# Optimization experiments

Measured on AMD Instinct MI355X. Metric: run time of the kernel, lower is better.

## Reference

```python
import jax, jax.numpy as jnp
import numpy as np

N, E, G = 100000, 1600000, 128
IN_DIM, H, C = 329, 4, 64
NEG_SLOPE = 0.2


def setup_inputs() -> dict:
    key = jax.random.key(0)
    ks = jax.random.split(key, 12)
    x = jax.random.normal(ks[0], (N, IN_DIM), dtype=jnp.float32)
    edge_index = jax.random.randint(ks[1], (2, E), 0, N, dtype=jnp.int64)
    batch = jnp.sort(jax.random.randint(ks[2], (N,), 0, G, dtype=jnp.int64))
    s = 1.0 / np.sqrt(IN_DIM)
    W = jax.random.uniform(ks[3], (IN_DIM, H * C), jnp.float32, -s, s)
    att_src = jax.random.normal(ks[4], (H, C), dtype=jnp.float32) * 0.1
    att_dst = jax.random.normal(ks[5], (H, C), dtype=jnp.float32) * 0.1
    bias = jnp.zeros((C,), jnp.float32)
    s1 = 1.0 / np.sqrt(C)
    w1 = jax.random.uniform(ks[6], (C, 64), jnp.float32, -s1, s1)
    b1 = jnp.zeros((64,), jnp.float32)
    s2 = 1.0 / np.sqrt(64)
    w2 = jax.random.uniform(ks[7], (64, 1), jnp.float32, -s2, s2)
    b2 = jnp.zeros((1,), jnp.float32)
    return {"x": x, "W": W, "att_src": att_src, "att_dst": att_dst,
            "bias": bias, "w1": w1, "b1": b1, "w2": w2, "b2": b2,
            "edge_index": edge_index, "batch": batch}


def reference(x, W, att_src, att_dst, bias, w1, b1, w2, b2, edge_index, batch):
    # --- GATConv (heads=4, concat=False, add_self_loops=True) ---
    xp = (x @ W).reshape(N, H, C)                       # [N,H,C]
    a_src = jnp.einsum('nhc,hc->nh', xp, att_src)       # [N,H]
    a_dst = jnp.einsum('nhc,hc->nh', xp, att_dst)       # [N,H]
    loops = jnp.arange(N, dtype=edge_index.dtype)
    src = jnp.concatenate([edge_index[0], loops])       # [E+N]
    dst = jnp.concatenate([edge_index[1], loops])
    logits = jax.nn.leaky_relu(a_src[src] + a_dst[dst], NEG_SLOPE)  # [E+N,H]
    # segment softmax over edges sharing a destination
    mx = jax.ops.segment_max(logits, dst, num_segments=N)
    ex = jnp.exp(logits - mx[dst])
    denom = jax.ops.segment_sum(ex, dst, num_segments=N)
    alpha = ex / denom[dst]                             # [E+N,H]
    msg = xp[src] * alpha[:, :, None]                   # [E+N,H,C]
    agg = jax.ops.segment_sum(msg, dst, num_segments=N) # [N,H,C]
    h = jax.nn.relu(agg.mean(axis=1) + bias)            # [N,C]
    # --- global mean pool over graphs ---
    counts = jax.ops.segment_sum(jnp.ones((N,), h.dtype), batch, num_segments=G)
    g = jax.ops.segment_sum(h, batch, num_segments=G) / jnp.maximum(counts, 1.0)[:, None]
    # --- head MLP ---
    y = jax.nn.sigmoid(jax.nn.relu(g @ w1 + b1) @ w2 + b2)  # [G,1]
    return y
```

## Files before the change

### kernel.cpp

```cpp
#include <hip/hip_runtime.h>
#include <math.h>

#define N_NODES 100000
#define N_EDGES 1600000
#define N_GRAPHS 128
#define IN_DIM 329
#define NH 4
#define CC 64
#define HC 256
#define NEG_SLOPE 0.2f
#define LOG2E 1.44269504f

#define K_PAD 384
#define M_PAD 100096
#define XBYTES (N_NODES * IN_DIM * 4)
#define NBUCK 196
#define BCAP 10240
#define EPB 8192

typedef unsigned short u16;
typedef unsigned char u8;
typedef unsigned int u32;
typedef __attribute__((ext_vector_type(8))) short short8;
typedef __attribute__((ext_vector_type(4))) float floatx4;
typedef __attribute__((ext_vector_type(2))) float floatx2;

__device__ __forceinline__ u16 f2bf(float f) {
    u32 u = __float_as_uint(f);
    u32 r = (u + 0x7FFFu + ((u >> 16) & 1u)) >> 16;
    return (u16)r;
}

__device__ __forceinline__ u32 pkbf(float a, float b) {
    return __builtin_amdgcn_perm(__float_as_uint(b), __float_as_uint(a), 0x07060302u);
}

__device__ __forceinline__ u8 f2fp8(float f) {
#if __has_builtin(__builtin_amdgcn_cvt_pk_fp8_f32)
    int pk = __builtin_amdgcn_cvt_pk_fp8_f32(f, f, 0, false);
    return (u8)(pk & 0xFF);
#else
    u32 u = __float_as_uint(f);
    u32 sgn = (u >> 24) & 0x80;
    float af = fabsf(f);
    if (af >= 448.f) return (u8)(sgn | 0x7E);
    if (af < 0.015625f) {
        int m = (int)rintf(af * 512.f);
        if (m >= 8) return (u8)(sgn | 0x08);
        return (u8)(sgn | (u32)m);
    }
    u32 au = u & 0x7FFFFFFF;
    u32 r = au + 0x0007FFFFu + ((au >> 20) & 1u);
    u32 e = r >> 23;
    u32 m3 = (r >> 20) & 7;
    int fe = (int)e - 127 + 7;
    if (fe >= 16) return (u8)(sgn | 0x7E);
    return (u8)(sgn | ((u32)fe << 3) | m3);
#endif
}

__device__ __forceinline__ float fp82f_sw(u32 b) {
    u32 s = (b & 0x80u) << 24;
    u32 e = (b >> 3) & 0xF;
    u32 m = b & 7;
    if (e == 0) {
        float v = (float)m * 0.001953125f;
        return (b & 0x80) ? -v : v;
    }
    return __uint_as_float(s | ((e + 120) << 23) | (m << 20));
}

__device__ __forceinline__ floatx4 dec4(int p) {
#if __has_builtin(__builtin_amdgcn_cvt_pk_f32_fp8)
    floatx2 lo = __builtin_amdgcn_cvt_pk_f32_fp8(p, false);
    floatx2 hi = __builtin_amdgcn_cvt_pk_f32_fp8(p, true);
    floatx4 r; r.x = lo.x; r.y = lo.y; r.z = hi.x; r.w = hi.y;
    return r;
#else
    floatx4 r;
    r.x = fp82f_sw(p & 0xFF);  r.y = fp82f_sw((p >> 8) & 0xFF);
    r.z = fp82f_sw((p >> 16) & 0xFF); r.w = fp82f_sw((p >> 24) & 0xFF);
    return r;
#endif
}

__device__ __forceinline__ void async_copy16(const void* g, void* l) {
    __builtin_amdgcn_global_load_lds((const __attribute__((address_space(1))) void*)g,
                                     (__attribute__((address_space(3))) void*)l, 16, 0, 0);
}

__global__ __launch_bounds__(256) void convw_kernel(const float* __restrict__ W, u16* __restrict__ WbT)
{
    int i = blockIdx.x * 256 + threadIdx.x;
    if (i >= HC * 96) return;
    int c = i / 96;
    int k0 = (i - c * 96) * 4;
    ushort4 o = {0, 0, 0, 0};
    const float* wp = W + c;
    if (k0 < IN_DIM)     o.x = f2bf(wp[(size_t)k0 * HC]);
    if (k0 + 1 < IN_DIM) o.y = f2bf(wp[(size_t)(k0 + 1) * HC]);
    if (k0 + 2 < IN_DIM) o.z = f2bf(wp[(size_t)(k0 + 2) * HC]);
    if (k0 + 3 < IN_DIM) o.w = f2bf(wp[(size_t)(k0 + 3) * HC]);
    *(ushort4*)(WbT + (size_t)c * K_PAD + k0) = o;
}

__global__ __launch_bounds__(512, 6) void gemm_mfma_kernel(
    const float* __restrict__ x, const u16* __restrict__ WbT, u8* __restrict__ xp8)
{
    __shared__ __align__(16) float Asf[64 * 64];
    __shared__ __align__(16) u16   Bs[256 * 64];

    const int tid = threadIdx.x;
    const int lane = tid & 63;
    const int wave = tid >> 6;
    const int lr = lane & 15;
    const int q = lane >> 4;
    const int row0 = blockIdx.x * 64;
    const int rm0 = (wave & 1) * 32;
    const int cn0 = (wave >> 1) * 64;

    floatx4 acc[2][4];
#pragma unroll
    for (int i = 0; i < 2; i++)
#pragma unroll
        for (int j = 0; j < 4; j++) {
            acc[i][j].x = 0.f; acc[i][j].y = 0.f; acc[i][j].z = 0.f; acc[i][j].w = 0.f;
        }

    for (int k0 = 0; k0 < K_PAD; k0 += 64) {
#pragma unroll
        for (int t = 0; t < 2; t++) {
            int chunk = tid + t * 512;
            int row = chunk >> 4, ch = chunk & 15;
            int chl = ch ^ (row & 15);
            long gb = (long)(row0 + row) * (IN_DIM * 4) + (long)k0 * 4 + chl * 16;
            if (gb > (long)XBYTES - 16) gb = (long)XBYTES - 16;
            async_copy16((const char*)x + gb, (char*)Asf + (size_t)chunk * 16);
        }
#pragma unroll
        for (int t = 0; t < 4; t++) {
            int off = (tid + t * 512) * 16;
            int rowb = off >> 7;
            int colb = off & 127;
            int gcol = colb ^ ((rowb & 7) * 16);
            const char* gb = (const char*)WbT + (size_t)rowb * (K_PAD * 2) + k0 * 2 + gcol;
            async_copy16(gb, (char*)Bs + off);
        }
        asm volatile("s_waitcnt vmcnt(0)" ::: "memory");
        __syncthreads();

#pragma unroll
        for (int ks = 0; ks < 2; ks++) {
            short8 af[2], bf[4];
#pragma unroll
            for (int i = 0; i < 2; i++) {
                int ra = rm0 + i * 16 + lr;
                int c0 = ks * 8 + q * 2;
                int sw = ra & 15;
                const float4* base = (const float4*)(Asf + ra * 64);
                float4 lo = base[c0 ^ sw];
                float4 hi = base[(c0 ^ sw) ^ 1];
                union { short8 v; u32 w[4]; } fr;
                fr.w[0] = pkbf(lo.x, lo.y);
                fr.w[1] = pkbf(lo.z, lo.w);
                fr.w[2] = pkbf(hi.x, hi.y);
                fr.w[3] = pkbf(hi.z, hi.w);
                af[i] = fr.v;
            }
#pragma unroll
            for (int j = 0; j < 4; j++) {
                int rb = cn0 + j * 16 + lr;
                int cb = (ks * 64 + q * 16) ^ ((rb & 7) * 16);
                bf[j] = *(const short8*)((const char*)Bs + rb * 128 + cb);
            }
#pragma unroll
            for (int i = 0; i < 2; i++)
#pragma unroll
                for (int j = 0; j < 4; j++)
                    acc[i][j] = __builtin_amdgcn_mfma_f32_16x16x32_bf16(af[i], bf[j], acc[i][j], 0, 0, 0);
        }
        __syncthreads();
    }

#pragma unroll
    for (int i = 0; i < 2; i++) {
#pragma unroll
        for (int j = 0; j < 4; j++) {
            int col = cn0 + j * 16 + lr;
            float v[4] = {acc[i][j].x, acc[i][j].y, acc[i][j].z, acc[i][j].w};
#pragma unroll
            for (int r = 0; r < 4; r++) {
                int row = row0 + rm0 + i * 16 + q * 4 + r;
                if (row < N_NODES) xp8[(size_t)row * HC + col] = f2fp8(v[r]);
            }
        }
    }
}

__global__ __launch_bounds__(256) void a8_kernel(
    const u8* __restrict__ xp8, const float* __restrict__ att_src, const float* __restrict__ att_dst,
    float* __restrict__ a_src, float* __restrict__ a_dst)
{
    int n = blockIdx.x * 4 + (threadIdx.x >> 6);
    int lane = threadIdx.x & 63;
    if (n >= N_NODES) return;
    int h = lane >> 4;
    int c0 = (lane & 15) * 4;
    int p = *(const int*)(xp8 + (size_t)n * HC + h * CC + c0);
    floatx4 v = dec4(p);
    const float* as = att_src + h * CC + c0;
    const float* ad = att_dst + h * CC + c0;
    float ps = v.x * as[0] + v.y * as[1] + v.z * as[2] + v.w * as[3];
    float pd = v.x * ad[0] + v.y * ad[1] + v.z * ad[2] + v.w * ad[3];
#pragma unroll
    for (int m = 1; m < 16; m <<= 1) {
        ps += __shfl_xor(ps, m, 64);
        pd += __shfl_xor(pd, m, 64);
    }
    if ((lane & 15) == 0) {
        a_src[n * 4 + h] = ps * LOG2E;
        a_dst[n * 4 + h] = pd * LOG2E;
    }
}

__global__ __launch_bounds__(256) void bin2_kernel(
    const int* __restrict__ ei, int* __restrict__ bcur, int2* __restrict__ bins)
{
    __shared__ int hist[NBUCK];
    __shared__ int gpos[NBUCK];
    __shared__ int lcur[NBUCK];
    __shared__ int sc[256];

    const int t = threadIdx.x;
    const int lo = blockIdx.x * EPB;
    const int hi = min(lo + EPB, N_EDGES + N_NODES);

    for (int b = t; b < NBUCK; b += 256) hist[b] = 0;
    __syncthreads();

    for (int i = lo + t; i < hi; i += 256) {
        int d = (i < N_EDGES) ? ei[N_EDGES + i] : (i - N_EDGES);
        atomicAdd(&hist[d >> 9], 1);
    }
    __syncthreads();

    int v = (t < NBUCK) ? hist[t] : 0;
    if (t < NBUCK) { gpos[t] = atomicAdd(&bcur[t], v); lcur[t] = 0; }
    (void)sc;
    __syncthreads();

    for (int i = lo + t; i < hi; i += 256) {
        int s, d;
        if (i < N_EDGES) { s = ei[i]; d = ei[N_EDGES + i]; }
        else             { s = i - N_EDGES; d = s; }
        int b = d >> 9;
        int pos = gpos[b] + atomicAdd(&lcur[b], 1);
        if (pos < BCAP) {
            int2 r; r.x = s; r.y = d;
            bins[(size_t)b * BCAP + pos] = r;
        }
    }
}

__global__ __launch_bounds__(512) void fill3_kernel(
    const int* __restrict__ bcur, const int2* __restrict__ bins,
    int2* __restrict__ rs_deg, int* __restrict__ csr)
{
    __shared__ int deg[512];
    __shared__ int cur[512];
    __shared__ int sc[256];
    __shared__ int order[BCAP];

    const int t = threadIdx.x;
    const int b = blockIdx.x;
    const int cnt = min(bcur[b], BCAP);
    const int2* bp = bins + (size_t)b * BCAP;
    const int gbase = b * BCAP;

    deg[t] = 0;
    __syncthreads();
    for (int i = t; i < cnt; i += 512) atomicAdd(&deg[bp[i].y & 511], 1);
    __syncthreads();

    int d0 = 0, d1 = 0;
    if (t < 256) {
        d0 = deg[2 * t]; d1 = deg[2 * t + 1];
        sc[t] = d0 + d1;
    }
    __syncthreads();
    for (int off = 1; off < 256; off <<= 1) {
        int u = (t < 256 && t >= off) ? sc[t - off] : 0;
        __syncthreads();
        if (t < 256) sc[t] += u;
        __syncthreads();
    }
    if (t < 256) {
        int excl = sc[t] - (d0 + d1);
        cur[2 * t] = excl;
        cur[2 * t + 1] = excl + d0;
        int n0 = b * 512 + 2 * t;
        if (n0 < N_NODES)     { int2 rd; rd.x = gbase + excl;      rd.y = d0; rs_deg[n0] = rd; }
        if (n0 + 1 < N_NODES) { int2 rd; rd.x = gbase + excl + d0; rd.y = d1; rs_deg[n0 + 1] = rd; }
    }
    __syncthreads();

    for (int i = t; i < cnt; i += 512) {
        int2 r = bp[i];
        int pos = atomicAdd(&cur[r.y & 511], 1);
        order[pos] = r.x;
    }
    __syncthreads();

    for (int i = t; i < cnt; i += 512) csr[gbase + i] = order[i];
}

__global__ __launch_bounds__(256) void aggregate_kernel(
    const u8* __restrict__ xp8, const float* __restrict__ a_src, const float* __restrict__ a_dst,
    const int2* __restrict__ rs_deg, const int* __restrict__ csr,
    const float* __restrict__ bias, float* __restrict__ hbuf)
{
    int n = blockIdx.x * 4 + (threadIdx.x >> 6);
    int lane = threadIdx.x & 63;
    if (n >= N_NODES) return;
    int2 rd = rs_deg[n];
    int rstart = __builtin_amdgcn_readfirstlane(rd.x);
    int deg    = __builtin_amdgcn_readfirstlane(rd.y);
    const int* ep = csr + rstart;
    int h = lane >> 4;
    int xoff = lane * 4;

    float ad = a_dst[n * 4 + h];

    const int dm1 = deg - 1;
    const int nb  = (deg + 3) >> 2;

    float acc0 = 0.f, acc1 = 0.f, acc2 = 0.f, acc3 = 0.f, den = 0.f;

    int iA0, iA1, iA2, iA3;
    int iB0 = 0, iB1 = 0, iB2 = 0, iB3 = 0;
    float aa0, aa1, aa2, aa3;  int pa0, pa1, pa2, pa3;
    float ab0, ab1, ab2, ab3;  int pb0, pb1, pb2, pb3;

#define AGG_LDI(eb_, j0, j1, j2, j3) do { \
        j0 = ep[min((eb_), dm1)];     j1 = ep[min((eb_) + 1, dm1)]; \
        j2 = ep[min((eb_) + 2, dm1)]; j3 = ep[min((eb_) + 3, dm1)]; } while (0)

#define AGG_LDD(j0, j1, j2, j3, a0_, a1_, a2_, a3_, q0_, q1_, q2_, q3_) do { \
        a0_ = a_src[(size_t)(j0) * 4 + h];  q0_ = *(const int*)(xp8 + (size_t)(j0) * HC + xoff); \
        a1_ = a_src[(size_t)(j1) * 4 + h];  q1_ = *(const int*)(xp8 + (size_t)(j1) * HC + xoff); \
        a2_ = a_src[(size_t)(j2) * 4 + h];  q2_ = *(const int*)(xp8 + (size_t)(j2) * HC + xoff); \
        a3_ = a_src[(size_t)(j3) * 4 + h];  q3_ = *(const int*)(xp8 + (size_t)(j3) * HC + xoff); } while (0)

#define AGG_CMP(eb_, a0_, a1_, a2_, a3_, q0_, q1_, q2_, q3_) do { \
        float z0 = a0_ + ad, z1 = a1_ + ad, z2 = a2_ + ad, z3 = a3_ + ad; \
        float w0 = exp2f(fmaxf(z0, NEG_SLOPE * z0)); \
        float w1 = exp2f(fmaxf(z1, NEG_SLOPE * z1)); \
        float w2 = exp2f(fmaxf(z2, NEG_SLOPE * z2)); \
        float w3 = exp2f(fmaxf(z3, NEG_SLOPE * z3)); \
        if ((eb_) + 3 >= deg) {                \
            if ((eb_) + 1 >= deg) w1 = 0.f; \
            if ((eb_) + 2 >= deg) w2 = 0.f; \
            if ((eb_) + 3 >= deg) w3 = 0.f; \
        } \
        den += (w0 + w1) + (w2 + w3); \
        floatx4 v0 = dec4(q0_), v1 = dec4(q1_), v2 = dec4(q2_), v3 = dec4(q3_); \
        acc0 = fmaf(w0, v0.x, acc0); acc1 = fmaf(w0, v0.y, acc1); \
        acc2 = fmaf(w0, v0.z, acc2); acc3 = fmaf(w0, v0.w, acc3); \
        acc0 = fmaf(w1, v1.x, acc0); acc1 = fmaf(w1, v1.y, acc1); \
        acc2 = fmaf(w1, v1.z, acc2); acc3 = fmaf(w1, v1.w, acc3); \
        acc0 = fmaf(w2, v2.x, acc0); acc1 = fmaf(w2, v2.y, acc1); \
        acc2 = fmaf(w2, v2.z, acc2); acc3 = fmaf(w2, v2.w, acc3); \
        acc0 = fmaf(w3, v3.x, acc0); acc1 = fmaf(w3, v3.y, acc1); \
        acc2 = fmaf(w3, v3.z, acc2); acc3 = fmaf(w3, v3.w, acc3); } while (0)

    AGG_LDI(0, iA0, iA1, iA2, iA3);
    AGG_LDD(iA0, iA1, iA2, iA3, aa0, aa1, aa2, aa3, pa0, pa1, pa2, pa3);
    if (nb > 1) AGG_LDI(4, iB0, iB1, iB2, iB3);

    for (int b = 0; b < nb; b += 2) {
        int eb = b * 4;
        if (b + 1 < nb) AGG_LDD(iB0, iB1, iB2, iB3, ab0, ab1, ab2, ab3, pb0, pb1, pb2, pb3);
        if (b + 2 < nb) AGG_LDI(eb + 8, iA0, iA1, iA2, iA3);
        AGG_CMP(eb, aa0, aa1, aa2, aa3, pa0, pa1, pa2, pa3);
        if (b + 1 < nb) {
            if (b + 2 < nb) AGG_LDD(iA0, iA1, iA2, iA3, aa0, aa1, aa2, aa3, pa0, pa1, pa2, pa3);
            if (b + 3 < nb) AGG_LDI(eb + 12, iB0, iB1, iB2, iB3);
            AGG_CMP(eb + 4, ab0, ab1, ab2, ab3, pb0, pb1, pb2, pb3);
        }
    }

#undef AGG_LDI
#undef AGG_LDD
#undef AGG_CMP

    float r = 1.f / den;
    acc0 *= r; acc1 *= r; acc2 *= r; acc3 *= r;
#pragma unroll
    for (int m = 16; m <= 32; m <<= 1) {
        acc0 += __shfl_xor(acc0, m, 64);
        acc1 += __shfl_xor(acc1, m, 64);
        acc2 += __shfl_xor(acc2, m, 64);
        acc3 += __shfl_xor(acc3, m, 64);
    }
    if (lane < 16) {
        const float* bp = bias + lane * 4;
        float4 o;
        o.x = fmaxf(0.25f * acc0 + bp[0], 0.f);
        o.y = fmaxf(0.25f * acc1 + bp[1], 0.f);
        o.z = fmaxf(0.25f * acc2 + bp[2], 0.f);
        o.w = fmaxf(0.25f * acc3 + bp[3], 0.f);
        *(float4*)&hbuf[(size_t)n * CC + lane * 4] = o;
    }
}

__global__ __launch_bounds__(256) void pool1_kernel(
    const float* __restrict__ hbuf, const int* __restrict__ batch,
    float* __restrict__ gsum, int* __restrict__ gcnt)
{
    int w = threadIdx.x >> 6, lane = threadIdx.x & 63;
    int r0 = blockIdx.x * 128 + w * 32;
    if (r0 >= N_NODES) return;
    int r1 = min(r0 + 32, N_NODES);
    int cur = batch[r0];
    float s = 0.f;
    int c = 0;
    for (int r = r0; r < r1; r++) {
        int bb = batch[r];
        if (bb != cur) {
            atomicAdd(&gsum[cur * 64 + lane], s);
            if (lane == 0) atomicAdd(&gcnt[cur], c);
            s = 0.f; c = 0; cur = bb;
        }
        s += hbuf[(size_t)r * CC + lane];
        c++;
    }
    atomicAdd(&gsum[cur * 64 + lane], s);
    if (lane == 0) atomicAdd(&gcnt[cur], c);
}

__global__ __launch_bounds__(64) void pool2_kernel(
    const float* __restrict__ gsum, const int* __restrict__ gcnt,
    const float* __restrict__ w1, const float* __restrict__ b1,
    const float* __restrict__ w2, const float* __restrict__ b2,
    float* __restrict__ out)
{
    int g = blockIdx.x;
    int lane = threadIdx.x;
    __shared__ float gv[64];
    gv[lane] = gsum[g * 64 + lane] / (float)max(gcnt[g], 1);
    __syncthreads();
    float hid = b1[lane];
    for (int c = 0; c < 64; c++) hid = fmaf(gv[c], w1[c * 64 + lane], hid);
    hid = fmaxf(hid, 0.f);
    float part = hid * w2[lane];
#pragma unroll
    for (int off = 32; off > 0; off >>= 1) part += __shfl_xor(part, off, 64);
    if (lane == 0) out[g] = 1.f / (1.f + __expf(-(part + b2[0])));
}

extern "C" void kernel_launch(void* const* d_in, const int* in_sizes, int n_in,
                              void* d_out, int out_size, void* d_ws, size_t ws_size,
                              hipStream_t stream)
{
    const float* x       = (const float*)d_in[0];
    const float* W       = (const float*)d_in[1];
    const float* att_src = (const float*)d_in[2];
    const float* att_dst = (const float*)d_in[3];
    const float* bias    = (const float*)d_in[4];
    const float* w1      = (const float*)d_in[5];
    const float* b1      = (const float*)d_in[6];
    const float* w2      = (const float*)d_in[7];
    const float* b2      = (const float*)d_in[8];
    const int*   ei      = (const int*)d_in[9];
    const int*   batch   = (const int*)d_in[10];
    float* out = (float*)d_out;

    char* ws = (char*)d_ws;
    size_t off = 0;
    auto alloc = [&](size_t bytes) -> void* {
        void* p = ws + off;
        off += (bytes + 255) & ~(size_t)255;
        return p;
    };
    u16*   WbT       = (u16*)alloc((size_t)HC * K_PAD * 2);
    u8*    xp8       = (u8*)alloc((size_t)N_NODES * HC);
    float* a_src_b   = (float*)alloc((size_t)N_NODES * NH * 4);
    float* a_dst_b   = (float*)alloc((size_t)N_NODES * NH * 4);
    size_t zoff0 = off;
    int*   bcur      = (int*)alloc((size_t)NBUCK * 4);
    float* gsum      = (float*)alloc((size_t)N_GRAPHS * 64 * 4);
    int*   gcnt      = (int*)alloc((size_t)N_GRAPHS * 4);
    size_t zbytes = off - zoff0;
    int2*  bins      = (int2*)alloc((size_t)NBUCK * BCAP * 8);
    int2*  rs_deg    = (int2*)alloc((size_t)N_NODES * 8);
    int*   csr       = (int*)alloc((size_t)NBUCK * BCAP * 4);
    float* hbuf      = (float*)alloc((size_t)N_NODES * CC * 4);

    hipMemsetAsync(bcur, 0, zbytes, stream);

    convw_kernel<<<(HC * 96 + 255) / 256, 256, 0, stream>>>(W, WbT);

    gemm_mfma_kernel<<<M_PAD / 64, 512, 0, stream>>>(x, WbT, xp8);

    a8_kernel<<<(N_NODES + 3) / 4, 256, 0, stream>>>(xp8, att_src, att_dst, a_src_b, a_dst_b);

    int tot = N_EDGES + N_NODES;
    bin2_kernel<<<(tot + EPB - 1) / EPB, 256, 0, stream>>>(ei, bcur, bins);
    fill3_kernel<<<NBUCK, 512, 0, stream>>>(bcur, bins, rs_deg, csr);

    aggregate_kernel<<<(N_NODES + 3) / 4, 256, 0, stream>>>(xp8, a_src_b, a_dst_b,
                                                            rs_deg, csr, bias, hbuf);

    pool1_kernel<<<(N_NODES + 127) / 128, 256, 0, stream>>>(hbuf, batch, gsum, gcnt);
    pool2_kernel<<<N_GRAPHS, 64, 0, stream>>>(gsum, gcnt, w1, b1, w2, b2, out);
}
```

Baseline: 403.0 us.

## Fuse attention-score dots into GEMM epilogue and pooling into aggregation

The attention dot products are now computed from the fp32 MFMA accumulators in the GEMM epilogue, which removes the separate a8 kernel and its re-read of xp8. The aggregate kernel also does the global mean-pool sum directly: it accumulates into shared memory when all four nodes in a block share a graph, and otherwise uses global atomics. This drops the hbuf write/read and the pool1 kernel. The cost is extra shuffles and registers in the GEMM, and a block-wide sync in the aggregate kernel. The attention scores are now taken from unquantized values rather than fp8, so they shift slightly.

```diff
diff --git a/kernel.cpp b/kernel.cpp
--- a/kernel.cpp
+++ b/kernel.cpp
@@ -105,7 +105,9 @@
 }
 
 __global__ __launch_bounds__(512, 6) void gemm_mfma_kernel(
-    const float* __restrict__ x, const u16* __restrict__ WbT, u8* __restrict__ xp8)
+    const float* __restrict__ x, const u16* __restrict__ WbT, u8* __restrict__ xp8,
+    const float* __restrict__ att_src, const float* __restrict__ att_dst,
+    float* __restrict__ a_src, float* __restrict__ a_dst)
 {
     __shared__ __align__(16) float Asf[64 * 64];
     __shared__ __align__(16) u16   Bs[256 * 64];
@@ -195,31 +197,48 @@
             }
         }
     }
-}
-
-__global__ __launch_bounds__(256) void a8_kernel(
-    const u8* __restrict__ xp8, const float* __restrict__ att_src, const float* __restrict__ att_dst,
-    float* __restrict__ a_src, float* __restrict__ a_dst)
-{
-    int n = blockIdx.x * 4 + (threadIdx.x >> 6);
-    int lane = threadIdx.x & 63;
-    if (n >= N_NODES) return;
-    int h = lane >> 4;
-    int c0 = (lane & 15) * 4;
-    int p = *(const int*)(xp8 + (size_t)n * HC + h * CC + c0);
-    floatx4 v = dec4(p);
-    const float* as = att_src + h * CC + c0;
-    const float* ad = att_dst + h * CC + c0;
-    float ps = v.x * as[0] + v.y * as[1] + v.z * as[2] + v.w * as[3];
-    float pd = v.x * ad[0] + v.y * ad[1] + v.z * ad[2] + v.w * ad[3];
+
+    float as0 = att_src[cn0 + 0 * 16 + lr], ad0 = att_dst[cn0 + 0 * 16 + lr];
+    float as1 = att_src[cn0 + 1 * 16 + lr], ad1 = att_dst[cn0 + 1 * 16 + lr];
+    float as2 = att_src[cn0 + 2 * 16 + lr], ad2 = att_dst[cn0 + 2 * 16 + lr];
+    float as3 = att_src[cn0 + 3 * 16 + lr], ad3 = att_dst[cn0 + 3 * 16 + lr];
+
+    float ps[2][4], pd[2][4];
+#pragma unroll
+    for (int i = 0; i < 2; i++) {
+        ps[i][0] = acc[i][0].x * as0 + acc[i][1].x * as1 + acc[i][2].x * as2 + acc[i][3].x * as3;
+        ps[i][1] = acc[i][0].y * as0 + acc[i][1].y * as1 + acc[i][2].y * as2 + acc[i][3].y * as3;
+        ps[i][2] = acc[i][0].z * as0 + acc[i][1].z * as1 + acc[i][2].z * as2 + acc[i][3].z * as3;
+        ps[i][3] = acc[i][0].w * as0 + acc[i][1].w * as1 + acc[i][2].w * as2 + acc[i][3].w * as3;
+        pd[i][0] = acc[i][0].x * ad0 + acc[i][1].x * ad1 + acc[i][2].x * ad2 + acc[i][3].x * ad3;
+        pd[i][1] = acc[i][0].y * ad0 + acc[i][1].y * ad1 + acc[i][2].y * ad2 + acc[i][3].y * ad3;
+        pd[i][2] = acc[i][0].z * ad0 + acc[i][1].z * ad1 + acc[i][2].z * ad2 + acc[i][3].z * ad3;
+        pd[i][3] = acc[i][0].w * ad0 + acc[i][1].w * ad1 + acc[i][2].w * ad2 + acc[i][3].w * ad3;
+    }
 #pragma unroll
     for (int m = 1; m < 16; m <<= 1) {
-        ps += __shfl_xor(ps, m, 64);
-        pd += __shfl_xor(pd, m, 64);
-    }
-    if ((lane & 15) == 0) {
-        a_src[n * 4 + h] = ps * LOG2E;
-        a_dst[n * 4 + h] = pd * LOG2E;
+#pragma unroll
+        for (int i = 0; i < 2; i++) {
+#pragma unroll
+            for (int r = 0; r < 4; r++) {
+                ps[i][r] += __shfl_xor(ps[i][r], m, 64);
+                pd[i][r] += __shfl_xor(pd[i][r], m, 64);
+            }
+        }
+    }
+    if (lr == 0) {
+        int head = wave >> 1;
+#pragma unroll
+        for (int i = 0; i < 2; i++) {
+#pragma unroll
+            for (int r = 0; r < 4; r++) {
+                int row = row0 + rm0 + i * 16 + q * 4 + r;
+                if (row < N_NODES) {
+                    a_src[row * 4 + head] = ps[i][r] * LOG2E;
+                    a_dst[row * 4 + head] = pd[i][r] * LOG2E;
+                }
+            }
+        }
     }
 }
 
@@ -317,11 +336,15 @@
 __global__ __launch_bounds__(256) void aggregate_kernel(
     const u8* __restrict__ xp8, const float* __restrict__ a_src, const float* __restrict__ a_dst,
     const int2* __restrict__ rs_deg, const int* __restrict__ csr,
-    const float* __restrict__ bias, float* __restrict__ hbuf)
-{
-    int n = blockIdx.x * 4 + (threadIdx.x >> 6);
+    const float* __restrict__ bias, const int* __restrict__ batch,
+    float* __restrict__ gsum, int* __restrict__ gcnt)
+{
+    __shared__ float gacc[64];
+    __shared__ int gids[4];
+
+    int w = threadIdx.x >> 6;
+    int n = blockIdx.x * 4 + w;
     int lane = threadIdx.x & 63;
-    if (n >= N_NODES) return;
     int2 rd = rs_deg[n];
     int rstart = __builtin_amdgcn_readfirstlane(rd.x);
     int deg    = __builtin_amdgcn_readfirstlane(rd.y);
@@ -402,40 +425,38 @@
         acc2 += __shfl_xor(acc2, m, 64);
         acc3 += __shfl_xor(acc3, m, 64);
     }
+
+    int g = batch[n];
+    if (threadIdx.x < 64) gacc[threadIdx.x] = 0.f;
+    if (lane == 0) gids[w] = g;
+    __syncthreads();
+    bool uni = (gids[0] == gids[1]) && (gids[1] == gids[2]) && (gids[2] == gids[3]);
+
     if (lane < 16) {
         const float* bp = bias + lane * 4;
-        float4 o;
-        o.x = fmaxf(0.25f * acc0 + bp[0], 0.f);
-        o.y = fmaxf(0.25f * acc1 + bp[1], 0.f);
-        o.z = fmaxf(0.25f * acc2 + bp[2], 0.f);
-        o.w = fmaxf(0.25f * acc3 + bp[3], 0.f);
-        *(float4*)&hbuf[(size_t)n * CC + lane * 4] = o;
-    }
-}
-
-__global__ __launch_bounds__(256) void pool1_kernel(
-    const float* __restrict__ hbuf, const int* __restrict__ batch,
-    float* __restrict__ gsum, int* __restrict__ gcnt)
-{
-    int w = threadIdx.x >> 6, lane = threadIdx.x & 63;
-    int r0 = blockIdx.x * 128 + w * 32;
-    if (r0 >= N_NODES) return;
-    int r1 = min(r0 + 32, N_NODES);
-    int cur = batch[r0];
-    float s = 0.f;
-    int c = 0;
-    for (int r = r0; r < r1; r++) {
-        int bb = batch[r];
-        if (bb != cur) {
-            atomicAdd(&gsum[cur * 64 + lane], s);
-            if (lane == 0) atomicAdd(&gcnt[cur], c);
-            s = 0.f; c = 0; cur = bb;
-        }
-        s += hbuf[(size_t)r * CC + lane];
-        c++;
-    }
-    atomicAdd(&gsum[cur * 64 + lane], s);
-    if (lane == 0) atomicAdd(&gcnt[cur], c);
+        float o0 = fmaxf(0.25f * acc0 + bp[0], 0.f);
+        float o1 = fmaxf(0.25f * acc1 + bp[1], 0.f);
+        float o2 = fmaxf(0.25f * acc2 + bp[2], 0.f);
+        float o3 = fmaxf(0.25f * acc3 + bp[3], 0.f);
+        if (uni) {
+            atomicAdd(&gacc[lane * 4 + 0], o0);
+            atomicAdd(&gacc[lane * 4 + 1], o1);
+            atomicAdd(&gacc[lane * 4 + 2], o2);
+            atomicAdd(&gacc[lane * 4 + 3], o3);
+        } else {
+            float* gp = gsum + (size_t)g * 64 + lane * 4;
+            atomicAdd(gp + 0, o0);
+            atomicAdd(gp + 1, o1);
+            atomicAdd(gp + 2, o2);
+            atomicAdd(gp + 3, o3);
+            if (lane == 0) atomicAdd(&gcnt[g], 1);
+        }
+    }
+    __syncthreads();
+    if (uni) {
+        if (threadIdx.x < 64) atomicAdd(&gsum[(size_t)gids[0] * 64 + threadIdx.x], gacc[threadIdx.x]);
+        if (threadIdx.x == 0) atomicAdd(&gcnt[gids[0]], 4);
+    }
 }
 
 __global__ __launch_bounds__(64) void pool2_kernel(
@@ -494,23 +515,21 @@
     int2*  bins      = (int2*)alloc((size_t)NBUCK * BCAP * 8);
     int2*  rs_deg    = (int2*)alloc((size_t)N_NODES * 8);
     int*   csr       = (int*)alloc((size_t)NBUCK * BCAP * 4);
-    float* hbuf      = (float*)alloc((size_t)N_NODES * CC * 4);
 
     hipMemsetAsync(bcur, 0, zbytes, stream);
 
     convw_kernel<<<(HC * 96 + 255) / 256, 256, 0, stream>>>(W, WbT);
 
-    gemm_mfma_kernel<<<M_PAD / 64, 512, 0, stream>>>(x, WbT, xp8);
-
-    a8_kernel<<<(N_NODES + 3) / 4, 256, 0, stream>>>(xp8, att_src, att_dst, a_src_b, a_dst_b);
+    gemm_mfma_kernel<<<M_PAD / 64, 512, 0, stream>>>(x, WbT, xp8, att_src, att_dst,
+                                                     a_src_b, a_dst_b);
 
     int tot = N_EDGES + N_NODES;
     bin2_kernel<<<(tot + EPB - 1) / EPB, 256, 0, stream>>>(ei, bcur, bins);
     fill3_kernel<<<NBUCK, 512, 0, stream>>>(bcur, bins, rs_deg, csr);
 
-    aggregate_kernel<<<(N_NODES + 3) / 4, 256, 0, stream>>>(xp8, a_src_b, a_dst_b,
-                                                            rs_deg, csr, bias, hbuf);
-
-    pool1_kernel<<<(N_NODES + 127) / 128, 256, 0, stream>>>(hbuf, batch, gsum, gcnt);
+    aggregate_kernel<<<N_NODES / 4, 256, 0, stream>>>(xp8, a_src_b, a_dst_b,
+                                                      rs_deg, csr, bias, batch,
+                                                      gsum, gcnt);
+
     pool2_kernel<<<N_GRAPHS, 64, 0, stream>>>(gsum, gcnt, w1, b1, w2, b2, out);
 }
```

New measurement: 464.0 us. 1.15x slower.

## Fuse attention logits into GEMM epilogue and merge edge binning into GEMM launch

Applied to the files above, without the earlier changes.

Computes per-node attention source/destination scores directly from the fp32 GEMM accumulators using lane shuffles, removing the separate pass that re-read the fp8 projected features. Also adds extra blocks to the GEMM grid that perform edge binning, so binning runs concurrently with the matrix multiply instead of as its own launch. This trades extra registers and shuffles in the GEMM epilogue and mixes heterogeneous block types in one grid, which may affect occupancy. Scores are now computed from unquantized values, slightly changing numerics.

```diff
diff --git a/kernel.cpp b/kernel.cpp
--- a/kernel.cpp
+++ b/kernel.cpp
@@ -17,6 +17,8 @@
 #define NBUCK 196
 #define BCAP 10240
 #define EPB 8192
+#define BIN_BLOCKS 208
+#define GEMM_BLOCKS (M_PAD / 64)
 
 typedef unsigned short u16;
 typedef unsigned char u8;
@@ -104,18 +106,59 @@
     *(ushort4*)(WbT + (size_t)c * K_PAD + k0) = o;
 }
 
-__global__ __launch_bounds__(512, 6) void gemm_mfma_kernel(
-    const float* __restrict__ x, const u16* __restrict__ WbT, u8* __restrict__ xp8)
+__global__ __launch_bounds__(512, 6) void gemm_bin_kernel(
+    const float* __restrict__ x, const u16* __restrict__ WbT, u8* __restrict__ xp8,
+    const float* __restrict__ att_src, const float* __restrict__ att_dst,
+    float* __restrict__ a_src, float* __restrict__ a_dst,
+    const int* __restrict__ ei, int* __restrict__ bcur, int2* __restrict__ bins)
 {
     __shared__ __align__(16) float Asf[64 * 64];
     __shared__ __align__(16) u16   Bs[256 * 64];
+    __shared__ int hist[NBUCK];
+    __shared__ int gpos[NBUCK];
+    __shared__ int lcur[NBUCK];
 
     const int tid = threadIdx.x;
+
+    if (blockIdx.x < BIN_BLOCKS) {
+        const int lo = blockIdx.x * EPB;
+        const int hi = min(lo + EPB, N_EDGES + N_NODES);
+
+        for (int b = tid; b < NBUCK; b += 512) hist[b] = 0;
+        __syncthreads();
+
+        for (int i = lo + tid; i < hi; i += 512) {
+            int d = (i < N_EDGES) ? ei[N_EDGES + i] : (i - N_EDGES);
+            atomicAdd(&hist[d >> 9], 1);
+        }
+        __syncthreads();
+
+        if (tid < NBUCK) {
+            int v = hist[tid];
+            gpos[tid] = atomicAdd(&bcur[tid], v);
+            lcur[tid] = 0;
+        }
+        __syncthreads();
+
+        for (int i = lo + tid; i < hi; i += 512) {
+            int s, d;
+            if (i < N_EDGES) { s = ei[i]; d = ei[N_EDGES + i]; }
+            else             { s = i - N_EDGES; d = s; }
+            int b = d >> 9;
+            int pos = gpos[b] + atomicAdd(&lcur[b], 1);
+            if (pos < BCAP) {
+                int2 r; r.x = s; r.y = d;
+                bins[(size_t)b * BCAP + pos] = r;
+            }
+        }
+        return;
+    }
+
     const int lane = tid & 63;
     const int wave = tid >> 6;
     const int lr = lane & 15;
     const int q = lane >> 4;
-    const int row0 = blockIdx.x * 64;
+    const int row0 = (blockIdx.x - BIN_BLOCKS) * 64;
     const int rm0 = (wave & 1) * 32;
     const int cn0 = (wave >> 1) * 64;
 
@@ -195,69 +238,47 @@
             }
         }
     }
-}
-
-__global__ __launch_bounds__(256) void a8_kernel(
-    const u8* __restrict__ xp8, const float* __restrict__ att_src, const float* __restrict__ att_dst,
-    float* __restrict__ a_src, float* __restrict__ a_dst)
-{
-    int n = blockIdx.x * 4 + (threadIdx.x >> 6);
-    int lane = threadIdx.x & 63;
-    if (n >= N_NODES) return;
-    int h = lane >> 4;
-    int c0 = (lane & 15) * 4;
-    int p = *(const int*)(xp8 + (size_t)n * HC + h * CC + c0);
-    floatx4 v = dec4(p);
-    const float* as = att_src + h * CC + c0;
-    const float* ad = att_dst + h * CC + c0;
-    float ps = v.x * as[0] + v.y * as[1] + v.z * as[2] + v.w * as[3];
-    float pd = v.x * ad[0] + v.y * ad[1] + v.z * ad[2] + v.w * ad[3];
+
+    float as0 = att_src[cn0 + 0 * 16 + lr], ad0 = att_dst[cn0 + 0 * 16 + lr];
+    float as1 = att_src[cn0 + 1 * 16 + lr], ad1 = att_dst[cn0 + 1 * 16 + lr];
+    float as2 = att_src[cn0 + 2 * 16 + lr], ad2 = att_dst[cn0 + 2 * 16 + lr];
+    float as3 = att_src[cn0 + 3 * 16 + lr], ad3 = att_dst[cn0 + 3 * 16 + lr];
+
+    float ps[2][4], pd[2][4];
+#pragma unroll
+    for (int i = 0; i < 2; i++) {
+        ps[i][0] = acc[i][0].x * as0 + acc[i][1].x * as1 + acc[i][2].x * as2 + acc[i][3].x * as3;
+        ps[i][1] = acc[i][0].y * as0 + acc[i][1].y * as1 + acc[i][2].y * as2 + acc[i][3].y * as3;
+        ps[i][2] = acc[i][0].z * as0 + acc[i][1].z * as1 + acc[i][2].z * as2 + acc[i][3].z * as3;
+        ps[i][3] = acc[i][0].w * as0 + acc[i][1].w * as1 + acc[i][2].w * as2 + acc[i][3].w * as3;
+        pd[i][0] = acc[i][0].x * ad0 + acc[i][1].x * ad1 + acc[i][2].x * ad2 + acc[i][3].x * ad3;
+        pd[i][1] = acc[i][0].y * ad0 + acc[i][1].y * ad1 + acc[i][2].y * ad2 + acc[i][3].y * ad3;
+        pd[i][2] = acc[i][0].z * ad0 + acc[i][1].z * ad1 + acc[i][2].z * ad2 + acc[i][3].z * ad3;
+        pd[i][3] = acc[i][0].w * ad0 + acc[i][1].w * ad1 + acc[i][2].w * ad2 + acc[i][3].w * ad3;
+    }
 #pragma unroll
     for (int m = 1; m < 16; m <<= 1) {
-        ps += __shfl_xor(ps, m, 64);
-        pd += __shfl_xor(pd, m, 64);
-    }
-    if ((lane & 15) == 0) {
-        a_src[n * 4 + h] = ps * LOG2E;
-        a_dst[n * 4 + h] = pd * LOG2E;
-    }
-}
-
-__global__ __launch_bounds__(256) void bin2_kernel(
-    const int* __restrict__ ei, int* __restrict__ bcur, int2* __restrict__ bins)
-{
-    __shared__ int hist[NBUCK];
-    __shared__ int gpos[NBUCK];
-    __shared__ int lcur[NBUCK];
-    __shared__ int sc[256];
-
-    const int t = threadIdx.x;
-    const int lo = blockIdx.x * EPB;
-    const int hi = min(lo + EPB, N_EDGES + N_NODES);
-
-    for (int b = t; b < NBUCK; b += 256) hist[b] = 0;
-    __syncthreads();
-
-    for (int i = lo + t; i < hi; i += 256) {
-        int d = (i < N_EDGES) ? ei[N_EDGES + i] : (i - N_EDGES);
-        atomicAdd(&hist[d >> 9], 1);
-    }
-    __syncthreads();
-
-    int v = (t < NBUCK) ? hist[t] : 0;
-    if (t < NBUCK) { gpos[t] = atomicAdd(&bcur[t], v); lcur[t] = 0; }
-    (void)sc;
-    __syncthreads();
-
-    for (int i = lo + t; i < hi; i += 256) {
-        int s, d;
-        if (i < N_EDGES) { s = ei[i]; d = ei[N_EDGES + i]; }
-        else             { s = i - N_EDGES; d = s; }
-        int b = d >> 9;
-        int pos = gpos[b] + atomicAdd(&lcur[b], 1);
-        if (pos < BCAP) {
-            int2 r; r.x = s; r.y = d;
-            bins[(size_t)b * BCAP + pos] = r;
+#pragma unroll
+        for (int i = 0; i < 2; i++) {
+#pragma unroll
+            for (int r = 0; r < 4; r++) {
+                ps[i][r] += __shfl_xor(ps[i][r], m, 64);
+                pd[i][r] += __shfl_xor(pd[i][r], m, 64);
+            }
+        }
+    }
+    if (lr == 0) {
+        int head = wave >> 1;
+#pragma unroll
+        for (int i = 0; i < 2; i++) {
+#pragma unroll
+            for (int r = 0; r < 4; r++) {
+                int row = row0 + rm0 + i * 16 + q * 4 + r;
+                if (row < N_NODES) {
+                    a_src[row * 4 + head] = ps[i][r] * LOG2E;
+                    a_dst[row * 4 + head] = pd[i][r] * LOG2E;
+                }
+            }
         }
     }
 }
@@ -500,12 +521,9 @@
 
     convw_kernel<<<(HC * 96 + 255) / 256, 256, 0, stream>>>(W, WbT);
 
-    gemm_mfma_kernel<<<M_PAD / 64, 512, 0, stream>>>(x, WbT, xp8);
-
-    a8_kernel<<<(N_NODES + 3) / 4, 256, 0, stream>>>(xp8, att_src, att_dst, a_src_b, a_dst_b);
-
-    int tot = N_EDGES + N_NODES;
-    bin2_kernel<<<(tot + EPB - 1) / EPB, 256, 0, stream>>>(ei, bcur, bins);
+    gemm_bin_kernel<<<BIN_BLOCKS + GEMM_BLOCKS, 512, 0, stream>>>(
+        x, WbT, xp8, att_src, att_dst, a_src_b, a_dst_b, ei, bcur, bins);
+
     fill3_kernel<<<NBUCK, 512, 0, stream>>>(bcur, bins, rs_deg, csr);
 
     aggregate_kernel<<<(N_NODES + 3) / 4, 256, 0, stream>>>(xp8, a_src_b, a_dst_b,
```

Measured after the change: 384.0 us. 4.7% less time.
